# Kernel tuning notes

Measured on AMD Instinct MI355X. Metric: run time of the kernel, lower is better.

Reference implementation:

```python
import jax, jax.numpy as jnp
import numpy as np

EPS = 0.1        # entropic regularization (init eps)
MAX_ITER = 100   # init max_iter
THRESH = 0.1     # early-stop threshold from original code
NORM_EPS = 1e-8


def setup_inputs() -> dict:
    key = jax.random.key(0)
    kx, ky = jax.random.split(key)
    x = jax.random.normal(kx, (16, 1024, 256), dtype=jnp.float32)
    y = jax.random.normal(ky, (16, 1024, 256), dtype=jnp.float32)
    return {"x": x, "y": y}


def _mfa_cost(x, y):
    # Cosine cost: E = 1 - cos(x_i, y_j), computed via normalized matmul
    # (norms clamped at 1e-8 as in torch CosineSimilarity).
    xn = x / jnp.maximum(jnp.linalg.norm(x, axis=-1, keepdims=True), NORM_EPS)
    yn = y / jnp.maximum(jnp.linalg.norm(y, axis=-1, keepdims=True), NORM_EPS)
    E = 1.0 - jnp.einsum('bnd,bmd->bnm', xn, yn)  # [B, N, M]

    B, N, M = E.shape
    log_mu = jnp.full((B, N), jnp.log(1.0 / N + 1e-8), dtype=E.dtype)
    log_nu = jnp.full((B, M), jnp.log(1.0 / M + 1e-8), dtype=E.dtype)

    def Mmat(u, v):
        # (-E + u_i + v_j) / eps, broadcast over [B, N, M]
        return (-E + u[..., :, None] + v[..., None, :]) / EPS

    @jax.checkpoint
    def body(carry, _):
        u, v, done = carry
        u_new = EPS * (log_mu - jax.nn.logsumexp(Mmat(u, v), axis=-1)) + u
        # original transposes then logsumexp over -1 == logsumexp over -2
        v_new = EPS * (log_nu - jax.nn.logsumexp(Mmat(u_new, v), axis=-2)) + v
        err = jnp.abs(u_new - u).sum(-1).mean()
        # emulate data-dependent break: freeze u, v once converged
        u_out = jnp.where(done, u, u_new)
        v_out = jnp.where(done, v, v_new)
        return (u_out, v_out, done | (err < THRESH)), None

    u0 = jnp.zeros((B, N), dtype=E.dtype)
    v0 = jnp.zeros((B, M), dtype=E.dtype)
    (u, v, _), _ = jax.lax.scan(body, (u0, v0, jnp.array(False)), None, length=MAX_ITER)

    pi = jnp.exp(Mmat(u, v))                 # transport plan [B, N, M]
    cost = jnp.sum(pi * E, axis=(-2, -1))    # [B]  (reduction='none')
    return cost


def reference(x, y):
    return _mfa_cost(x, y)
```

## Files before the change

### kernel.cpp

```cpp
#include <hip/hip_runtime.h>

typedef _Float16 half_t;
typedef __attribute__((ext_vector_type(8))) _Float16 half8;
typedef __attribute__((ext_vector_type(4))) float f32x4;
typedef __attribute__((ext_vector_type(8))) short short8v;
typedef unsigned short u16;
typedef unsigned int u32;

#define SCALE_F     14.4269504f
#define INV_SCALE_F 0.0693147181f
#define C_MU       -9.99998523f
#define C_NU       -9.99998523f
#define MU_F        0.000976572498f
#define ERR_STOP_B  1.44269504f
#define MAX_ITER    100
#define SPIN_LIMIT  50000000LL

#define SMEM_E   131072
#define SMEM_CP  16384
#define SMEM_V   4096
#define SMEM_RED 256
#define SMEM_TOTAL (SMEM_E + SMEM_CP + SMEM_V + SMEM_RED)

#define PSTRIDE  520

__device__ __forceinline__ float fexp2(float x) { return __builtin_amdgcn_exp2f(x); }
__device__ __forceinline__ float flog2(float x) { return __builtin_amdgcn_logf(x); }
__device__ __forceinline__ float frcp(float x)  { return __builtin_amdgcn_rcpf(x); }

__device__ __forceinline__ u16 f2bf(float f) {
  unsigned u = __float_as_uint(f);
  return (u16)((u + 0x7fffu + ((u >> 16) & 1u)) >> 16);
}
__device__ __forceinline__ float bf2f(u16 h) {
  return __uint_as_float(((unsigned)h) << 16);
}

__global__ __launch_bounds__(256) void mfa_prep(const float* __restrict__ x,
                                                const float* __restrict__ y,
                                                u16* __restrict__ Xn,
                                                u16* __restrict__ Yn,
                                                int* __restrict__ epoch,
                                                float* __restrict__ cost) {
  int g = blockIdx.x * 256 + threadIdx.x;
  if (g < 256) epoch[g] = 0;
  if (g < 16)  cost[g] = 0.0f;

  int wid = g >> 6;
  int lane = threadIdx.x & 63;
  for (int rr = 0; rr < 32; ++rr) {
    int row = wid + (rr << 10);
    const float* src = (row < 16384) ? x + (size_t)row * 256
                                     : y + (size_t)(row - 16384) * 256;
    float4 xa = ((const float4*)src)[lane];
    float ss = xa.x*xa.x + xa.y*xa.y + xa.z*xa.z + xa.w*xa.w;
    #pragma unroll
    for (int off = 32; off; off >>= 1) ss += __shfl_xor(ss, off);
    float inv = 1.0f / fmaxf(sqrtf(ss), 1e-8f);
    ushort4 o;
    o.x = f2bf(xa.x * inv); o.y = f2bf(xa.y * inv);
    o.z = f2bf(xa.z * inv); o.w = f2bf(xa.w * inv);
    u16* dst = ((row < 16384) ? Xn + ((size_t)row << 8)
                              : Yn + ((size_t)(row - 16384) << 8)) + lane * 4;
    *(ushort4*)dst = o;
  }
}

__global__ __launch_bounds__(512, 1) void mfa_sink_fused(
    const u16* __restrict__ Xn, const u16* __restrict__ Yn,
    u32* __restrict__ partials, int* __restrict__ epoch,
    float* __restrict__ cost) {
  extern __shared__ char smem[];
  half_t* Els  = (half_t*)smem;
  float*  cpb  = (float*)(smem + SMEM_E);
  float*  vsh  = (float*)(smem + SMEM_E + SMEM_CP);
  float*  sred = (float*)(smem + SMEM_E + SMEM_CP + SMEM_V);

  const int t = threadIdx.x, w = t >> 6, lane = t & 63;
  const int lane15 = lane & 15, lgrp = lane >> 4;
  const int blk = blockIdx.x;
  const int b = ((blk & 7) << 1) | ((blk >> 7) & 1);
  const int k = (blk >> 3) & 15;

  {
    const u16* Xb = Xn + ((size_t)((b << 10) + (k << 6)) << 8);
    const u16* Yb = Yn + ((size_t)(b << 10) << 8);
    const int wcol = w << 7;
    #pragma unroll
    for (int pass = 0; pass < 2; ++pass) {
      const int c0 = wcol + (pass << 6);
      f32x4 acc[4][4];
      #pragma unroll
      for (int i = 0; i < 4; ++i)
        #pragma unroll
        for (int j = 0; j < 4; ++j) acc[i][j] = (f32x4){0.f, 0.f, 0.f, 0.f};
      for (int ks = 0; ks < 8; ++ks) {
        const int koff = (ks << 5) + (lgrp << 3);
        short8v a[4], bb[4];
        #pragma unroll
        for (int i = 0; i < 4; ++i)
          a[i] = *(const short8v*)(Xb + (((i << 4) + lane15) << 8) + koff);
        #pragma unroll
        for (int j = 0; j < 4; ++j)
          bb[j] = *(const short8v*)(Yb + ((size_t)(c0 + (j << 4) + lane15) << 8) + koff);
        #pragma unroll
        for (int i = 0; i < 4; ++i)
          #pragma unroll
          for (int j = 0; j < 4; ++j)
            acc[i][j] = __builtin_amdgcn_mfma_f32_16x16x32_bf16(a[i], bb[j], acc[i][j], 0, 0, 0);
      }
      #pragma unroll
      for (int i = 0; i < 4; ++i)
        #pragma unroll
        for (int j = 0; j < 4; ++j) {
          const int col = c0 + (j << 4) + lane15;
          #pragma unroll
          for (int q = 0; q < 4; ++q) {
            const int row = (i << 4) + (lgrp << 2) + q;
            Els[(row << 10) + col] = (half_t)((1.0f - acc[i][j][q]) * SCALE_F);
          }
        }
    }
  }
  vsh[t] = 0.0f; vsh[t + 512] = 0.0f;
  __syncthreads();

  float ureg[8];
  #pragma unroll
  for (int r = 0; r < 8; ++r) ureg[r] = 0.0f;

  const int mlo = lane << 3;
  int it = 0;
  for (; it < MAX_ITER; ++it) {
    const f32x4* v4 = (const f32x4*)vsh;
    f32x4 va = v4[lane*2], vb = v4[lane*2 + 1];
    f32x4 vc = v4[128 + lane*2], vd = v4[128 + lane*2 + 1];
    float vv[16];
    vv[0]=va.x; vv[1]=va.y; vv[2]=va.z; vv[3]=va.w;
    vv[4]=vb.x; vv[5]=vb.y; vv[6]=vb.z; vv[7]=vb.w;
    vv[8]=vc.x; vv[9]=vc.y; vv[10]=vc.z; vv[11]=vc.w;
    vv[12]=vd.x; vv[13]=vd.y; vv[14]=vd.z; vv[15]=vd.w;

    float colacc[16];
    #pragma unroll
    for (int j = 0; j < 16; ++j) colacc[j] = 0.0f;
    float werr = 0.0f;

    #pragma unroll
    for (int r = 0; r < 8; ++r) {
      const half8* E8 = (const half8*)(Els + (((w << 3) + r) << 10));
      half8 ea = E8[lane], eb = E8[lane + 64];
      float rt[16];
      float s = 0.0f;
      #pragma unroll
      for (int j = 0; j < 8; ++j) { rt[j] = fexp2(vv[j] - (float)ea[j]); s += rt[j]; }
      #pragma unroll
      for (int j = 0; j < 8; ++j) { rt[8+j] = fexp2(vv[8+j] - (float)eb[j]); s += rt[8+j]; }
      #pragma unroll
      for (int off = 32; off; off >>= 1) s += __shfl_xor(s, off);
      float unew = C_MU - flog2(s);
      float eu = MU_F * frcp(s);
      werr += fabsf(unew - ureg[r]);
      ureg[r] = unew;
      #pragma unroll
      for (int j = 0; j < 16; ++j) colacc[j] += rt[j] * eu;
    }
    if (lane == 0) sred[w] = werr;

    if (w < 4) {
      #pragma unroll
      for (int j = 0; j < 4; ++j) {
        *(f32x4*)&cpb[w*1024 + mlo + 4*j - ((j>=2)?8:0) + ((j>=2)?512:0)] =
            (f32x4){colacc[4*j], colacc[4*j+1], colacc[4*j+2], colacc[4*j+3]};
      }
    }
    __syncthreads();
    if (w >= 4) {
      const int wb = (w - 4) * 1024;
      #pragma unroll
      for (int j = 0; j < 8; ++j) cpb[wb + mlo + j] += colacc[j];
      #pragma unroll
      for (int j = 0; j < 8; ++j) cpb[wb + 512 + mlo + j] += colacc[8 + j];
    }
    __syncthreads();

    const int p = it & 1;
    u32* ps = partials + (size_t)((((p << 4) | b) << 4) | k) * PSTRIDE;
    {
      float2 q0 = *(const float2*)&cpb[2*t];
      float2 q1 = *(const float2*)&cpb[1024 + 2*t];
      float2 q2 = *(const float2*)&cpb[2048 + 2*t];
      float2 q3 = *(const float2*)&cpb[3072 + 2*t];
      float ca = q0.x + q1.x + q2.x + q3.x;
      float cb = q0.y + q1.y + q2.y + q3.y;
      u32 packed = (u32)f2bf(ca) | ((u32)f2bf(cb) << 16);
      __hip_atomic_store(&ps[t], packed, __ATOMIC_RELAXED, __HIP_MEMORY_SCOPE_AGENT);
      if (t == 0) {
        float be = sred[0]+sred[1]+sred[2]+sred[3]+sred[4]+sred[5]+sred[6]+sred[7];
        __hip_atomic_store(&ps[512], __float_as_uint(be), __ATOMIC_RELAXED,
                           __HIP_MEMORY_SCOPE_AGENT);
      }
    }
    __syncthreads();

    if (t == 0) {
      __hip_atomic_store(&epoch[(b << 4) | k], it + 1, __ATOMIC_RELAXED,
                         __HIP_MEMORY_SCOPE_AGENT);
      long long t0c = clock64();
      for (;;) {
        int mn = 0x7fffffff;
        #pragma unroll
        for (int j = 0; j < 16; ++j) {
          int e = __hip_atomic_load(&epoch[(b << 4) | j], __ATOMIC_RELAXED,
                                    __HIP_MEMORY_SCOPE_AGENT);
          mn = min(mn, e);
        }
        if (mn >= it + 1) break;
        __builtin_amdgcn_s_sleep(1);
        if (clock64() - t0c > SPIN_LIMIT) break;
      }
    }
    __syncthreads();

    {
      const u32* pb32 = partials + (size_t)(((p << 4) | b) << 4) * PSTRIDE;
      float t0s = 0.0f, t1s = 0.0f;
      #pragma unroll
      for (int j = 0; j < 16; ++j) {
        u32 pw = __hip_atomic_load(&pb32[j * PSTRIDE + t], __ATOMIC_RELAXED,
                                   __HIP_MEMORY_SCOPE_AGENT);
        t0s += bf2f((u16)(pw & 0xffffu));
        t1s += bf2f((u16)(pw >> 16));
      }
      float we = 0.0f;
      if (t < 16)
        we = __uint_as_float(__hip_atomic_load(&pb32[t * PSTRIDE + 512],
                                               __ATOMIC_RELAXED,
                                               __HIP_MEMORY_SCOPE_AGENT));
      if (w == 0) {
        #pragma unroll
        for (int off = 8; off; off >>= 1) we += __shfl_xor(we, off);
        if (lane == 0) sred[8] = we;
      }
      float v0n = vsh[2*t]     + C_NU - flog2(t0s);
      float v1n = vsh[2*t + 1] + C_NU - flog2(t1s);
      vsh[2*t] = v0n; vsh[2*t + 1] = v1n;
    }
    __syncthreads();

    if (sred[8] < ERR_STOP_B) break;
  }

  {
    const f32x4* v4 = (const f32x4*)vsh;
    f32x4 va = v4[lane*2], vb = v4[lane*2 + 1];
    f32x4 vc = v4[128 + lane*2], vd = v4[128 + lane*2 + 1];
    float vv[16];
    vv[0]=va.x; vv[1]=va.y; vv[2]=va.z; vv[3]=va.w;
    vv[4]=vb.x; vv[5]=vb.y; vv[6]=vb.z; vv[7]=vb.w;
    vv[8]=vc.x; vv[9]=vc.y; vv[10]=vc.z; vv[11]=vc.w;
    vv[12]=vd.x; vv[13]=vd.y; vv[14]=vd.z; vv[15]=vd.w;
    float cacc = 0.0f;
    #pragma unroll
    for (int r = 0; r < 8; ++r) {
      const half8* E8 = (const half8*)(Els + (((w << 3) + r) << 10));
      half8 ea = E8[lane], eb = E8[lane + 64];
      float un = ureg[r];
      #pragma unroll
      for (int j = 0; j < 8; ++j) {
        float e = (float)ea[j];
        cacc += fexp2(un + vv[j] - e) * e;
      }
      #pragma unroll
      for (int j = 0; j < 8; ++j) {
        float e = (float)eb[j];
        cacc += fexp2(un + vv[8+j] - e) * e;
      }
    }
    #pragma unroll
    for (int off = 32; off; off >>= 1) cacc += __shfl_xor(cacc, off);
    if (lane == 0) sred[w] = cacc;
    __syncthreads();
    if (t == 0)
      atomicAdd(&cost[b], (sred[0]+sred[1]+sred[2]+sred[3]+sred[4]+sred[5]+
                           sred[6]+sred[7]) * INV_SCALE_F);
  }
}

extern "C" void kernel_launch(void* const* d_in, const int* in_sizes, int n_in,
                              void* d_out, int out_size, void* d_ws, size_t ws_size,
                              hipStream_t stream) {
  const float* x = (const float*)d_in[0];
  const float* y = (const float*)d_in[1];
  float* cost = (float*)d_out;

  char* base = (char*)d_ws;
  u16* Xn       = (u16*)base;
  u16* Yn       = (u16*)(base + 8388608);
  u32* partials = (u32*)(base + 16777216);
  char* pb = base + 16777216 + (size_t)2*16*16*PSTRIDE*4;
  int* epoch = (int*)pb;  pb += 256 * 4;
  if ((size_t)(pb - base) > ws_size) return;

  mfa_prep<<<256, 256, 0, stream>>>(x, y, Xn, Yn, epoch, cost);

  (void)hipFuncSetAttribute((const void*)mfa_sink_fused,
                            hipFuncAttributeMaxDynamicSharedMemorySize, SMEM_TOTAL);
  mfa_sink_fused<<<dim3(256), dim3(512), SMEM_TOTAL, stream>>>(
      Xn, Yn, partials, epoch, cost);
}
```

Measured before the change: 76.48 us.

## Replace epoch barrier with tag-stamped partials polled directly by consumers

Removes the per-iteration epoch counter barrier, where thread 0 spun on 16 epoch words and then two block syncs followed. Each partial word now carries a 2-bit iteration tag in its low mantissa bits, and every thread polls its own words until the tag matches. This cuts one round trip and a __syncthreads from the critical path. Partials are also stored as fp32 with truncated low bits instead of bf16, which doubles the partial traffic. Correctness relies on a relaxed load of the full word being tear-free and on the tag wrapping safely with double buffering.

```diff
diff --git a/kernel.cpp b/kernel.cpp
--- a/kernel.cpp
+++ b/kernel.cpp
@@ -22,7 +22,8 @@
 #define SMEM_RED 256
 #define SMEM_TOTAL (SMEM_E + SMEM_CP + SMEM_V + SMEM_RED)
 
-#define PSTRIDE  520
+#define PSTRIDE  1040
+#define PWORDS   (2*16*16*PSTRIDE)
 
 __device__ __forceinline__ float fexp2(float x) { return __builtin_amdgcn_exp2f(x); }
 __device__ __forceinline__ float flog2(float x) { return __builtin_amdgcn_logf(x); }
@@ -32,19 +33,27 @@
   unsigned u = __float_as_uint(f);
   return (u16)((u + 0x7fffu + ((u >> 16) & 1u)) >> 16);
 }
-__device__ __forceinline__ float bf2f(u16 h) {
-  return __uint_as_float(((unsigned)h) << 16);
+
+__device__ __forceinline__ u32 agload(const u32* p) {
+  return __hip_atomic_load(p, __ATOMIC_RELAXED, __HIP_MEMORY_SCOPE_AGENT);
+}
+__device__ __forceinline__ void agstore(u32* p, u32 v) {
+  __hip_atomic_store(p, v, __ATOMIC_RELAXED, __HIP_MEMORY_SCOPE_AGENT);
 }
 
 __global__ __launch_bounds__(256) void mfa_prep(const float* __restrict__ x,
                                                 const float* __restrict__ y,
                                                 u16* __restrict__ Xn,
                                                 u16* __restrict__ Yn,
-                                                int* __restrict__ epoch,
+                                                u32* __restrict__ partials,
                                                 float* __restrict__ cost) {
   int g = blockIdx.x * 256 + threadIdx.x;
-  if (g < 256) epoch[g] = 0;
-  if (g < 16)  cost[g] = 0.0f;
+  if (g < 16) cost[g] = 0.0f;
+  #pragma unroll
+  for (int j = 0; j < 9; ++j) {
+    int idx = (j << 16) + g;
+    if (idx < PWORDS) partials[idx] = 0u;
+  }
 
   int wid = g >> 6;
   int lane = threadIdx.x & 63;
@@ -68,8 +77,7 @@
 
 __global__ __launch_bounds__(512, 1) void mfa_sink_fused(
     const u16* __restrict__ Xn, const u16* __restrict__ Yn,
-    u32* __restrict__ partials, int* __restrict__ epoch,
-    float* __restrict__ cost) {
+    u32* __restrict__ partials, float* __restrict__ cost) {
   extern __shared__ char smem[];
   half_t* Els  = (half_t*)smem;
   float*  cpb  = (float*)(smem + SMEM_E);
@@ -133,13 +141,13 @@
   int it = 0;
   for (; it < MAX_ITER; ++it) {
     const f32x4* v4 = (const f32x4*)vsh;
-    f32x4 va = v4[lane*2], vb = v4[lane*2 + 1];
-    f32x4 vc = v4[128 + lane*2], vd = v4[128 + lane*2 + 1];
+    f32x4 va4 = v4[lane*2], vb4 = v4[lane*2 + 1];
+    f32x4 vc4 = v4[128 + lane*2], vd4 = v4[128 + lane*2 + 1];
     float vv[16];
-    vv[0]=va.x; vv[1]=va.y; vv[2]=va.z; vv[3]=va.w;
-    vv[4]=vb.x; vv[5]=vb.y; vv[6]=vb.z; vv[7]=vb.w;
-    vv[8]=vc.x; vv[9]=vc.y; vv[10]=vc.z; vv[11]=vc.w;
-    vv[12]=vd.x; vv[13]=vd.y; vv[14]=vd.z; vv[15]=vd.w;
+    vv[0]=va4.x; vv[1]=va4.y; vv[2]=va4.z; vv[3]=va4.w;
+    vv[4]=vb4.x; vv[5]=vb4.y; vv[6]=vb4.z; vv[7]=vb4.w;
+    vv[8]=vc4.x; vv[9]=vc4.y; vv[10]=vc4.z; vv[11]=vc4.w;
+    vv[12]=vd4.x; vv[13]=vd4.y; vv[14]=vd4.z; vv[15]=vd4.w;
 
     float colacc[16];
     #pragma unroll
@@ -185,66 +193,65 @@
     __syncthreads();
 
     const int p = it & 1;
-    u32* ps = partials + (size_t)((((p << 4) | b) << 4) | k) * PSTRIDE;
+    const u32 tag = (u32)((it + 1) & 3);
     {
+      u32* ps = partials + (size_t)((((p << 4) | b) << 4) | k) * PSTRIDE;
       float2 q0 = *(const float2*)&cpb[2*t];
       float2 q1 = *(const float2*)&cpb[1024 + 2*t];
       float2 q2 = *(const float2*)&cpb[2048 + 2*t];
       float2 q3 = *(const float2*)&cpb[3072 + 2*t];
       float ca = q0.x + q1.x + q2.x + q3.x;
       float cb = q0.y + q1.y + q2.y + q3.y;
-      u32 packed = (u32)f2bf(ca) | ((u32)f2bf(cb) << 16);
-      __hip_atomic_store(&ps[t], packed, __ATOMIC_RELAXED, __HIP_MEMORY_SCOPE_AGENT);
+      agstore(&ps[2*t],     (__float_as_uint(ca) & ~3u) | tag);
+      agstore(&ps[2*t + 1], (__float_as_uint(cb) & ~3u) | tag);
       if (t == 0) {
         float be = sred[0]+sred[1]+sred[2]+sred[3]+sred[4]+sred[5]+sred[6]+sred[7];
-        __hip_atomic_store(&ps[512], __float_as_uint(be), __ATOMIC_RELAXED,
-                           __HIP_MEMORY_SCOPE_AGENT);
-      }
-    }
-    __syncthreads();
-
-    if (t == 0) {
-      __hip_atomic_store(&epoch[(b << 4) | k], it + 1, __ATOMIC_RELAXED,
-                         __HIP_MEMORY_SCOPE_AGENT);
-      long long t0c = clock64();
-      for (;;) {
-        int mn = 0x7fffffff;
-        #pragma unroll
-        for (int j = 0; j < 16; ++j) {
-          int e = __hip_atomic_load(&epoch[(b << 4) | j], __ATOMIC_RELAXED,
-                                    __HIP_MEMORY_SCOPE_AGENT);
-          mn = min(mn, e);
-        }
-        if (mn >= it + 1) break;
-        __builtin_amdgcn_s_sleep(1);
-        if (clock64() - t0c > SPIN_LIMIT) break;
-      }
-    }
-    __syncthreads();
+        agstore(&ps[1024], (__float_as_uint(be) & ~3u) | tag);
+      }
+    }
 
     {
       const u32* pb32 = partials + (size_t)(((p << 4) | b) << 4) * PSTRIDE;
+      u32 wa[16], wb[16];
+      #pragma unroll
+      for (int j = 0; j < 16; ++j) {
+        wa[j] = agload(&pb32[j * PSTRIDE + 2*t]);
+        wb[j] = agload(&pb32[j * PSTRIDE + 2*t + 1]);
+      }
+      long long tws = clock64();
+      #pragma unroll
+      for (int j = 0; j < 16; ++j) {
+        while ((wa[j] & 3u) != tag) {
+          wa[j] = agload(&pb32[j * PSTRIDE + 2*t]);
+          if (clock64() - tws > SPIN_LIMIT) break;
+        }
+        while ((wb[j] & 3u) != tag) {
+          wb[j] = agload(&pb32[j * PSTRIDE + 2*t + 1]);
+          if (clock64() - tws > SPIN_LIMIT) break;
+        }
+      }
       float t0s = 0.0f, t1s = 0.0f;
       #pragma unroll
       for (int j = 0; j < 16; ++j) {
-        u32 pw = __hip_atomic_load(&pb32[j * PSTRIDE + t], __ATOMIC_RELAXED,
-                                   __HIP_MEMORY_SCOPE_AGENT);
-        t0s += bf2f((u16)(pw & 0xffffu));
-        t1s += bf2f((u16)(pw >> 16));
-      }
-      float we = 0.0f;
-      if (t < 16)
-        we = __uint_as_float(__hip_atomic_load(&pb32[t * PSTRIDE + 512],
-                                               __ATOMIC_RELAXED,
-                                               __HIP_MEMORY_SCOPE_AGENT));
+        t0s += __uint_as_float(wa[j]);
+        t1s += __uint_as_float(wb[j]);
+      }
       if (w == 0) {
+        float we = 0.0f;
+        if (lane < 16) {
+          u32 ww = agload(&pb32[lane * PSTRIDE + 1024]);
+          while ((ww & 3u) != tag) {
+            ww = agload(&pb32[lane * PSTRIDE + 1024]);
+            if (clock64() - tws > SPIN_LIMIT) break;
+          }
+          we = __uint_as_float(ww);
+        }
         #pragma unroll
         for (int off = 8; off; off >>= 1) we += __shfl_xor(we, off);
         if (lane == 0) sred[8] = we;
       }
-      float v0n = vsh[2*t]     + C_NU - flog2(t0s);
-      float v1n = vsh[2*t + 1] + C_NU - flog2(t1s);
-      vsh[2*t] = v0n; vsh[2*t + 1] = v1n;
+      vsh[2*t]     += C_NU - flog2(t0s);
+      vsh[2*t + 1] += C_NU - flog2(t1s);
     }
     __syncthreads();
 
@@ -253,13 +260,13 @@
 
   {
     const f32x4* v4 = (const f32x4*)vsh;
-    f32x4 va = v4[lane*2], vb = v4[lane*2 + 1];
-    f32x4 vc = v4[128 + lane*2], vd = v4[128 + lane*2 + 1];
+    f32x4 va4 = v4[lane*2], vb4 = v4[lane*2 + 1];
+    f32x4 vc4 = v4[128 + lane*2], vd4 = v4[128 + lane*2 + 1];
     float vv[16];
-    vv[0]=va.x; vv[1]=va.y; vv[2]=va.z; vv[3]=va.w;
-    vv[4]=vb.x; vv[5]=vb.y; vv[6]=vb.z; vv[7]=vb.w;
-    vv[8]=vc.x; vv[9]=vc.y; vv[10]=vc.z; vv[11]=vc.w;
-    vv[12]=vd.x; vv[13]=vd.y; vv[14]=vd.z; vv[15]=vd.w;
+    vv[0]=va4.x; vv[1]=va4.y; vv[2]=va4.z; vv[3]=va4.w;
+    vv[4]=vb4.x; vv[5]=vb4.y; vv[6]=vb4.z; vv[7]=vb4.w;
+    vv[8]=vc4.x; vv[9]=vc4.y; vv[10]=vc4.z; vv[11]=vc4.w;
+    vv[12]=vd4.x; vv[13]=vd4.y; vv[14]=vd4.z; vv[15]=vd4.w;
     float cacc = 0.0f;
     #pragma unroll
     for (int r = 0; r < 8; ++r) {
@@ -298,14 +305,13 @@
   u16* Xn       = (u16*)base;
   u16* Yn       = (u16*)(base + 8388608);
   u32* partials = (u32*)(base + 16777216);
-  char* pb = base + 16777216 + (size_t)2*16*16*PSTRIDE*4;
-  int* epoch = (int*)pb;  pb += 256 * 4;
-  if ((size_t)(pb - base) > ws_size) return;
-
-  mfa_prep<<<256, 256, 0, stream>>>(x, y, Xn, Yn, epoch, cost);
+  size_t needed = 16777216 + (size_t)PWORDS * 4;
+  if (ws_size < needed) return;
+
+  mfa_prep<<<256, 256, 0, stream>>>(x, y, Xn, Yn, partials, cost);
 
   (void)hipFuncSetAttribute((const void*)mfa_sink_fused,
                             hipFuncAttributeMaxDynamicSharedMemorySize, SMEM_TOTAL);
   mfa_sink_fused<<<dim3(256), dim3(512), SMEM_TOTAL, stream>>>(
-      Xn, Yn, partials, epoch, cost);
-}
+      Xn, Yn, partials, cost);
+}
```

Result: slower. 83.02 us (+8.5%).
